# Kernel optimization log

Measured on AMD Instinct MI355X. Metric: run time of the kernel, lower is better.

Reference implementation:

```python
import jax, jax.numpy as jnp
import numpy as np
import math

N_GENES_TOTAL = 20000
N_CELLS_TOTAL = 10000
N_LATENT = 64
N_COMP = 32
SCALE_LOWER_BOUND = 1e-5
LOG_2PI = math.log(2.0 * math.pi)


def setup_inputs() -> dict:
    key = jax.random.key(0)
    ks = jax.random.split(key, 16)
    n_cells, n_genes = 512, 4000
    n_cuts, n_frags = 1000000, 1000000
    inp = {}
    inp["local_cellxgene_ix"] = jax.random.randint(ks[0], (n_frags,), 0, n_cells * n_genes)
    inp["cut_coordinates"] = jax.random.uniform(ks[1], (n_cuts,), dtype=jnp.float32)
    inp["latent"] = jax.random.normal(ks[2], (n_cells, N_LATENT), dtype=jnp.float32)
    inp["genes_oi"] = jax.random.randint(ks[3], (n_genes,), 0, N_GENES_TOTAL)
    inp["cells_oi"] = jax.random.randint(ks[4], (n_cells,), 0, N_CELLS_TOTAL)
    inp["cut_local_cellxgene_ix"] = jax.random.randint(ks[5], (n_cuts,), 0, n_cells * n_genes)
    inp["cut_local_gene_ix"] = jax.random.randint(ks[6], (n_cuts,), 0, n_genes)
    inp["n_cells"] = n_cells
    inp["n_genes"] = n_genes
    # Mixture parameters (per total gene)
    loc_init = jnp.linspace(0.0, 1.0, N_COMP + 2)[1:-1]  # (C,)
    inp["loc_w"] = jnp.broadcast_to(jax.scipy.special.logit(loc_init), (N_GENES_TOTAL, N_COMP)).astype(jnp.float32)
    inp["scale_w"] = jnp.full((N_GENES_TOTAL, N_COMP), math.log(1.0 / N_COMP / 5.0), dtype=jnp.float32)
    inp["logit_w"] = (jax.random.normal(ks[7], (N_GENES_TOTAL, N_COMP)) / math.sqrt(N_COMP)).astype(jnp.float32)
    # Decoder sparse embeddings (n_layers=0 -> input dim = n_latent)
    stdv_l = 1.0 / math.sqrt(N_LATENT)
    inp["logit_weight"] = jax.random.uniform(ks[8], (N_GENES_TOTAL, N_LATENT, N_COMP), minval=-stdv_l, maxval=stdv_l, dtype=jnp.float32)
    stdv_r = 1.0 / math.sqrt(N_LATENT) / 100.0
    inp["rho_weight"] = jax.random.uniform(ks[9], (N_GENES_TOTAL, N_LATENT), minval=-stdv_r, maxval=stdv_r, dtype=jnp.float32)
    inp["rho_bias"] = jax.random.uniform(ks[10], (N_GENES_TOTAL,), minval=1e-4, maxval=1e-2, dtype=jnp.float32)
    inp["libsize"] = jax.random.uniform(ks[11], (N_CELLS_TOTAL,), minval=1000.0, maxval=10000.0, dtype=jnp.float32)
    return inp


def reference(local_cellxgene_ix, cut_coordinates, latent, genes_oi, cells_oi,
              cut_local_cellxgene_ix, cut_local_gene_ix, n_cells, n_genes,
              loc_w, scale_w, logit_w, logit_weight, rho_weight, rho_bias, libsize):
    # Decoder (n_layers=0 => nn_output == latent)
    lw = logit_weight[genes_oi]                      # [G, L, C]
    rw = rho_weight[genes_oi]                        # [G, L]
    mixture_delta = jnp.einsum("nl,glc->ngc", latent, lw)   # [N, G, C]
    rho = latent @ rw.T                               # [N, G]

    # Gather per-cut mixture delta
    C = mixture_delta.shape[-1]
    delta = mixture_delta.reshape(-1, C)[cut_local_cellxgene_ix]  # [K, C]

    # Mixture log prob
    loc = jax.nn.sigmoid(loc_w[genes_oi])[cut_local_gene_ix]                 # [K, C]
    scale = SCALE_LOWER_BOUND + jnp.exp(scale_w[genes_oi])[cut_local_gene_ix]  # [K, C]
    logits = logit_w[genes_oi][cut_local_gene_ix] + delta                    # [K, C]
    z = (cut_coordinates[:, None] - loc) / scale
    comp_lp = -0.5 * z * z - jnp.log(scale) - 0.5 * LOG_2PI                  # Normal log_prob
    likelihood_mixture = jax.scipy.special.logsumexp(jax.nn.log_softmax(logits, axis=-1) + comp_lp, axis=-1)  # [K]

    # Fragment count Poisson likelihood
    fragmentexpression = rho_bias[genes_oi][None, :] * jnp.exp(rho) * libsize[cells_oi][:, None]  # [N, G]
    counts = jnp.zeros((n_cells * n_genes,), dtype=jnp.float32).at[local_cellxgene_ix].add(1.0).reshape(n_cells, n_genes)
    likelihood_fragmentcounts = counts * jnp.log(fragmentexpression) - fragmentexpression - jax.lax.lgamma(counts + 1.0)

    elbo = -(likelihood_mixture.sum() + likelihood_fragmentcounts.sum())
    return elbo
```

## Files before the change

kernel.cpp:

```cpp
#include <hip/hip_runtime.h>


#define TPB 256
#define CHUNK 4096
#define MAXG 4096
#define MAXN 1024
#define HALF_LOG_2PI 0.9189385332046727f

typedef short bf16x8 __attribute__((ext_vector_type(8)));
typedef float f32x4 __attribute__((ext_vector_type(4)));

static __device__ __forceinline__ unsigned short f2bf(float f) {
  unsigned u = __float_as_uint(f);
  u += 0x7fffu + ((u >> 16) & 1u);
  return (unsigned short)(u >> 16);
}

static __device__ __forceinline__ float block_reduce(float v) {
  #pragma unroll
  for (int off = 32; off > 0; off >>= 1) v += __shfl_down(v, off, 64);
  __shared__ float wsum[4];
  if ((threadIdx.x & 63) == 0) wsum[threadIdx.x >> 6] = v;
  __syncthreads();
  return (threadIdx.x == 0) ? (wsum[0] + wsum[1] + wsum[2] + wsum[3]) : 0.f;
}

__global__ __launch_bounds__(TPB) void gene_params_kernel(
    const int* __restrict__ genes_oi,
    const float* __restrict__ loc_w, const float* __restrict__ scale_w,
    const float* __restrict__ logit_w,
    const float* __restrict__ latent,
    float4* __restrict__ gp, unsigned short* __restrict__ latbf,
    int G, int NL) {
  int idx = blockIdx.x * TPB + threadIdx.x;
  int ngp = G * 32;
  if (idx < ngp) {
    int g = idx >> 5, c = idx & 31;
    long long gene = genes_oi[g];
    float lv = loc_w[gene * 32 + c];
    float loc = 1.f / (1.f + __expf(-lv));
    float sc = 1e-5f + __expf(scale_w[gene * 32 + c]);
    gp[idx] = make_float4(loc, 1.f / sc, -__logf(sc) - HALF_LOG_2PI, logit_w[gene * 32 + c]);
  } else {
    int t = idx - ngp;
    if (t < NL) latbf[t] = f2bf(latent[t]);
  }
}

__global__ __launch_bounds__(TPB) void sort_pass1(
    const int* __restrict__ cxg, const int* __restrict__ lix,
    unsigned* __restrict__ cntC, unsigned* __restrict__ cntF,
    int K, int F, unsigned G, unsigned N) {
  __shared__ unsigned hC[MAXG];
  __shared__ unsigned hF[MAXN];
  for (int t = threadIdx.x; t < MAXG; t += TPB) hC[t] = 0;
  for (int t = threadIdx.x; t < MAXN; t += TPB) hF[t] = 0;
  __syncthreads();
  int i0 = blockIdx.x * CHUNK;
  for (int t = threadIdx.x; t < CHUNK; t += TPB) {
    int i = i0 + t;
    if (i < K) { unsigned ix = (unsigned)cxg[i]; atomicAdd(&hC[ix % G], 1u); }
    if (i < F) { unsigned v = (unsigned)lix[i]; atomicAdd(&hF[v / G], 1u); }
  }
  __syncthreads();
  size_t b = blockIdx.x;
  for (unsigned t = threadIdx.x; t < G; t += TPB) cntC[b * G + t] = hC[t];
  for (unsigned t = threadIdx.x; t < N; t += TPB) cntF[b * N + t] = hF[t];
}

__global__ __launch_bounds__(TPB) void colscan_kernel(
    unsigned* __restrict__ cntC, unsigned* __restrict__ cntF,
    unsigned* __restrict__ totC, unsigned* __restrict__ totF,
    int B, unsigned G, unsigned N) {
  unsigned t = blockIdx.x * TPB + threadIdx.x;
  if (t < G) {
    unsigned run = 0;
    for (int b = 0; b < B; b++) {
      unsigned v = cntC[(size_t)b * G + t];
      cntC[(size_t)b * G + t] = run;
      run += v;
    }
    totC[t] = run;
  } else if (t < G + N) {
    unsigned s = t - G;
    unsigned run = 0;
    for (int b = 0; b < B; b++) {
      unsigned v = cntF[(size_t)b * N + s];
      cntF[(size_t)b * N + s] = run;
      run += v;
    }
    totF[s] = run;
  }
}

static __device__ void scan_dev(const unsigned* __restrict__ cnt,
                                unsigned* __restrict__ offs, int S, unsigned M) {
  __shared__ unsigned tmp[TPB];
  __shared__ unsigned base;
  if (threadIdx.x == 0) base = 0;
  __syncthreads();
  for (int c0 = 0; c0 < S; c0 += TPB) {
    int i = c0 + (int)threadIdx.x;
    unsigned v = (i < S) ? cnt[i] : 0u;
    tmp[threadIdx.x] = v;
    __syncthreads();
    for (int d = 1; d < TPB; d <<= 1) {
      unsigned t = (threadIdx.x >= (unsigned)d) ? tmp[threadIdx.x - d] : 0u;
      __syncthreads();
      tmp[threadIdx.x] += t;
      __syncthreads();
    }
    unsigned excl = tmp[threadIdx.x] - v + base;
    if (i < S) offs[i] = excl;
    __syncthreads();
    if (threadIdx.x == TPB - 1) base = excl + v;
    __syncthreads();
  }
  if (threadIdx.x == 0) offs[S] = M;
  __syncthreads();
}

__global__ __launch_bounds__(TPB) void scan2_kernel(
    const unsigned* __restrict__ totC, unsigned* __restrict__ baseC, int SC, unsigned K,
    const unsigned* __restrict__ totF, unsigned* __restrict__ baseF, int SF, unsigned F) {
  scan_dev(totC, baseC, SC, K);
  scan_dev(totF, baseF, SF, F);
}

__global__ __launch_bounds__(TPB) void sort_pass3(
    const int* __restrict__ cxg, const int* __restrict__ lix,
    const float* __restrict__ xc, const int* __restrict__ gix,
    const unsigned* __restrict__ cntC, const unsigned* __restrict__ cntF,
    const unsigned* __restrict__ baseC, const unsigned* __restrict__ baseF,
    float2* __restrict__ pl, unsigned* __restrict__ fpl,
    int K, int F, unsigned G, unsigned N) {
  __shared__ unsigned cC[MAXG];
  __shared__ unsigned cF[MAXN];
  for (int t = threadIdx.x; t < MAXG; t += TPB) cC[t] = 0;
  for (int t = threadIdx.x; t < MAXN; t += TPB) cF[t] = 0;
  __syncthreads();
  int i0 = blockIdx.x * CHUNK;
  size_t b = blockIdx.x;
  for (int t = threadIdx.x; t < CHUNK; t += TPB) {
    int i = i0 + t;
    if (i < K) {
      unsigned ix = (unsigned)cxg[i];
      unsigned g = ix % G, n = ix / G;
      unsigned r = atomicAdd(&cC[g], 1u);
      unsigned pos = baseC[g] + cntC[b * G + g] + r;
      pl[pos] = make_float2(xc[i], __uint_as_float((n << 16) | (unsigned)gix[i]));
    }
    if (i < F) {
      unsigned v = (unsigned)lix[i];
      unsigned n = v / G, g = v - n * G;
      unsigned r = atomicAdd(&cF[n], 1u);
      fpl[baseF[n] + cntF[b * N + n] + r] = (n << 16) | g;
    }
  }
}

__global__ __launch_bounds__(TPB) void cuts_v6(
    const float2* __restrict__ pl, const unsigned short* __restrict__ latbf,
    const int* __restrict__ genes_oi, const float* __restrict__ logit_weight,
    const float4* __restrict__ gp, const unsigned* __restrict__ baseC,
    float* __restrict__ partials, unsigned G) {
  const int g = blockIdx.x;
  const int lane = threadIdx.x & 63;
  const int wv = threadIdx.x >> 6;
  const int quad = lane >> 4;
  const int r16 = lane & 15;

  const float* Wb = logit_weight + (size_t)genes_oi[g] * 2048;
  bf16x8 B0a, B1a, B0b, B1b;
  #pragma unroll
  for (int j = 0; j < 8; j++) {
    int l0 = quad * 8 + j;
    B0a[j] = (short)f2bf(Wb[l0 * 32 + r16]);
    B1a[j] = (short)f2bf(Wb[(l0 + 32) * 32 + r16]);
    B0b[j] = (short)f2bf(Wb[l0 * 32 + r16 + 16]);
    B1b[j] = (short)f2bf(Wb[(l0 + 32) * 32 + r16 + 16]);
  }

  const unsigned start = baseC[g], end = baseC[g + 1];
  const unsigned ntiles = (end - start + 15) >> 4;
  float lm = 0.f;

  for (unsigned t = wv; t < ntiles; t += 4) {
    unsigned kk0 = start + t * 16;
    unsigned idx = kk0 + r16;
    float2 p = pl[idx < end ? idx : start];
    unsigned u = __float_as_uint(p.y);
    const unsigned short* lb = latbf + (size_t)(u >> 16) * 64;
    bf16x8 A0 = *(const bf16x8*)(lb + quad * 8);
    bf16x8 A1 = *(const bf16x8*)(lb + 32 + quad * 8);

    f32x4 acc0 = {0.f, 0.f, 0.f, 0.f};
    f32x4 acc1 = {0.f, 0.f, 0.f, 0.f};
    acc0 = __builtin_amdgcn_mfma_f32_16x16x32_bf16(A0, B0a, acc0, 0, 0, 0);
    acc0 = __builtin_amdgcn_mfma_f32_16x16x32_bf16(A1, B1a, acc0, 0, 0, 0);
    acc1 = __builtin_amdgcn_mfma_f32_16x16x32_bf16(A0, B0b, acc1, 0, 0, 0);
    acc1 = __builtin_amdgcn_mfma_f32_16x16x32_bf16(A1, B1b, acc1, 0, 0, 0);

    #pragma unroll
    for (int r = 0; r < 4; r++) {
      int cut = quad * 4 + r;
      float xr = __shfl(p.x, cut, 64);
      unsigned ur = (unsigned)__shfl((int)u, cut, 64);
      unsigned gi = ur & 0xffffu;
      float4 q0 = gp[(size_t)gi * 32 + r16];
      float4 q1 = gp[(size_t)gi * 32 + r16 + 16];
      float t0 = q0.w + acc0[r], t1 = q1.w + acc1[r];
      float z0 = (xr - q0.x) * q0.y, z1 = (xr - q1.x) * q1.y;
      float u0 = t0 + fmaf(-0.5f * z0, z0, q0.z);
      float u1 = t1 + fmaf(-0.5f * z1, z1, q1.z);
      float e1 = __expf(u0) + __expf(u1);
      float e2 = __expf(t0) + __expf(t1);
      #pragma unroll
      for (int d = 1; d < 16; d <<= 1) {
        e1 += __shfl_xor(e1, d, 64);
        e2 += __shfl_xor(e2, d, 64);
      }
      if (r16 == 0 && (kk0 + (unsigned)cut) < end) lm += __logf(e1) - __logf(e2);
    }
  }
  float bs = block_reduce(lm);
  if (threadIdx.x == 0) partials[blockIdx.x] = bs;
}

__global__ __launch_bounds__(TPB) void pois_v4(
    const unsigned* __restrict__ fpl, const unsigned* __restrict__ baseF,
    const float* __restrict__ latent, const int* __restrict__ genes_oi,
    const int* __restrict__ cells_oi,
    const float* __restrict__ rho_weight, const float* __restrict__ rho_bias,
    const float* __restrict__ libsize,
    float* __restrict__ partials, int N, int G) {
  int n0 = blockIdx.x * 2;
  __shared__ unsigned cnt[2 * MAXG];
  for (int t = threadIdx.x; t < 2 * MAXG; t += TPB) cnt[t] = 0;
  __shared__ __align__(16) float lat[128];
  for (int t = threadIdx.x; t < 128; t += TPB) {
    int j = t >> 6, l = t & 63;
    lat[t] = (n0 + j < N) ? latent[(size_t)(n0 + j) * 64 + l] : 0.f;
  }
  __syncthreads();
  int nhi = min(n0 + 2, N);
  unsigned s0 = baseF[n0], e0 = baseF[nhi];
  for (unsigned i = s0 + threadIdx.x; i < e0; i += TPB) {
    unsigned v = fpl[i];
    unsigned j = (v >> 16) - (unsigned)n0, g = v & 0xffffu;
    atomicAdd(&cnt[j * MAXG + g], 1u);
  }
  __syncthreads();
  float lib0 = (n0 < N) ? libsize[cells_oi[n0]] : 0.f;
  float lib1 = (n0 + 1 < N) ? libsize[cells_oi[n0 + 1]] : 0.f;
  float sum = 0.f;
  for (int g = threadIdx.x; g < G; g += TPB) {
    long long gene = genes_oi[g];
    const float4* rw = (const float4*)(rho_weight + gene * 64);
    float r0 = 0.f, r1 = 0.f;
    #pragma unroll
    for (int i = 0; i < 16; i++) {
      float4 wv = rw[i];
      float4 l0 = *(const float4*)(&lat[i * 4]);
      float4 l1 = *(const float4*)(&lat[64 + i * 4]);
      r0 = fmaf(wv.x, l0.x, r0); r0 = fmaf(wv.y, l0.y, r0);
      r0 = fmaf(wv.z, l0.z, r0); r0 = fmaf(wv.w, l0.w, r0);
      r1 = fmaf(wv.x, l1.x, r1); r1 = fmaf(wv.y, l1.y, r1);
      r1 = fmaf(wv.z, l1.z, r1); r1 = fmaf(wv.w, l1.w, r1);
    }
    float rb = rho_bias[gene];
    if (n0 < N) {
      float fe = rb * __expf(r0) * lib0;
      unsigned c = cnt[g];
      float term = -fe;
      if (c) {
        float lf = 0.f;
        for (unsigned q2 = 2; q2 <= c; q2++) lf += __logf((float)q2);
        term += (float)c * __logf(fe) - lf;
      }
      sum += term;
    }
    if (n0 + 1 < N) {
      float fe = rb * __expf(r1) * lib1;
      unsigned c = cnt[MAXG + g];
      float term = -fe;
      if (c) {
        float lf = 0.f;
        for (unsigned q2 = 2; q2 <= c; q2++) lf += __logf((float)q2);
        term += (float)c * __logf(fe) - lf;
      }
      sum += term;
    }
  }
  float bs = block_reduce(sum);
  if (threadIdx.x == 0) partials[blockIdx.x] = bs;
}

__global__ __launch_bounds__(TPB) void finalize_kernel(
    const float* __restrict__ p1, int n1,
    const float* __restrict__ p2, int n2, float* __restrict__ out) {
  float s = 0.f;
  for (int i = threadIdx.x; i < n1; i += TPB) s += p1[i];
  for (int i = threadIdx.x; i < n2; i += TPB) s += p2[i];
  float bs = block_reduce(s);
  if (threadIdx.x == 0) out[0] = -bs;
}

extern "C" void kernel_launch(void* const* d_in, const int* in_sizes, int n_in,
                              void* d_out, int out_size, void* d_ws, size_t ws_size,
                              hipStream_t stream) {
  const int*   lix          = (const int*)d_in[0];
  const float* xc           = (const float*)d_in[1];
  const float* latent       = (const float*)d_in[2];
  const int*   genes_oi     = (const int*)d_in[3];
  const int*   cells_oi     = (const int*)d_in[4];
  const int*   cxg          = (const int*)d_in[5];
  const int*   gix          = (const int*)d_in[6];
  const float* loc_w        = (const float*)d_in[9];
  const float* scale_w      = (const float*)d_in[10];
  const float* logit_w      = (const float*)d_in[11];
  const float* logit_weight = (const float*)d_in[12];
  const float* rho_weight   = (const float*)d_in[13];
  const float* rho_bias     = (const float*)d_in[14];
  const float* libsize      = (const float*)d_in[15];
  float* out = (float*)d_out;

  const int F = in_sizes[0];
  const int K = in_sizes[1];
  const int N = in_sizes[2] / 64;
  const int G = in_sizes[3];
  const int NL = N * 64;

  const int M = (K > F) ? K : F;
  const int B = (M + CHUNK - 1) / CHUNK;
  const int PB = (N + 1) / 2;

  size_t off = 0;
  auto alloc = [&](size_t bytes) {
    size_t o = off;
    off = (off + bytes + 255) & ~(size_t)255;
    return o;
  };
  size_t cntC_off  = alloc((size_t)B * G * 4);
  size_t cntF_off  = alloc((size_t)B * N * 4);
  size_t totC_off  = alloc((size_t)G * 4);
  size_t totF_off  = alloc((size_t)N * 4);
  size_t baseC_off = alloc((size_t)(G + 1) * 4);
  size_t baseF_off = alloc((size_t)(N + 1) * 4);
  size_t pl_off    = alloc((size_t)K * 8);
  size_t fpl_off   = alloc((size_t)F * 4);
  size_t gp_off    = alloc((size_t)G * 32 * 16);
  size_t lb_off    = alloc((size_t)NL * 2);
  size_t p1_off    = alloc((size_t)G * 4);
  size_t p2_off    = alloc((size_t)PB * 4);
  (void)ws_size;

  char* ws = (char*)d_ws;
  unsigned* cntC  = (unsigned*)(ws + cntC_off);
  unsigned* cntF  = (unsigned*)(ws + cntF_off);
  unsigned* totC  = (unsigned*)(ws + totC_off);
  unsigned* totF  = (unsigned*)(ws + totF_off);
  unsigned* baseC = (unsigned*)(ws + baseC_off);
  unsigned* baseF = (unsigned*)(ws + baseF_off);
  float2*   pl    = (float2*)(ws + pl_off);
  unsigned* fpl   = (unsigned*)(ws + fpl_off);
  float4*   gp    = (float4*)(ws + gp_off);
  unsigned short* latbf = (unsigned short*)(ws + lb_off);
  float*    p1    = (float*)(ws + p1_off);
  float*    p2    = (float*)(ws + p2_off);

  gene_params_kernel<<<(G * 32 + NL + TPB - 1) / TPB, TPB, 0, stream>>>(
      genes_oi, loc_w, scale_w, logit_w, latent, gp, latbf, G, NL);
  sort_pass1<<<B, TPB, 0, stream>>>(cxg, lix, cntC, cntF, K, F, (unsigned)G, (unsigned)N);
  colscan_kernel<<<(G + N + TPB - 1) / TPB, TPB, 0, stream>>>(
      cntC, cntF, totC, totF, B, (unsigned)G, (unsigned)N);
  scan2_kernel<<<1, TPB, 0, stream>>>(totC, baseC, G, (unsigned)K, totF, baseF, N, (unsigned)F);
  sort_pass3<<<B, TPB, 0, stream>>>(cxg, lix, xc, gix, cntC, cntF, baseC, baseF,
                                    pl, fpl, K, F, (unsigned)G, (unsigned)N);
  cuts_v6<<<G, TPB, 0, stream>>>(pl, latbf, genes_oi, logit_weight, gp, baseC, p1, (unsigned)G);
  pois_v4<<<PB, TPB, 0, stream>>>(fpl, baseF, latent, genes_oi, cells_oi,
                                  rho_weight, rho_bias, libsize, p2, N, G);
  finalize_kernel<<<1, TPB, 0, stream>>>(p1, G, p2, PB, out);
}
```

Measured before the change: 533.6 us.

## Merge prep kernels, wave-parallel scans, and fold finalize into Poisson kernel

Fuses the gene-parameter/latent-conversion kernel into the first histogram pass as extra blocks, and rewrites the column scan so one wavefront scans each column with shuffles instead of one serial thread. The global scan now uses one wavefront per array with shuffle scans in place of a barrier-heavy block scan. The final reduction kernel is removed: the last Poisson block, found through an atomic ticket, sums all partials. This cuts kernel launches and serial scan latency, at the cost of a ticket reset and threadfence ordering.

```diff
diff --git a/kernel.cpp b/kernel.cpp
--- a/kernel.cpp
+++ b/kernel.cpp
@@ -25,32 +25,29 @@
   return (threadIdx.x == 0) ? (wsum[0] + wsum[1] + wsum[2] + wsum[3]) : 0.f;
 }
 
-__global__ __launch_bounds__(TPB) void gene_params_kernel(
+__global__ __launch_bounds__(TPB) void prep_hist_kernel(
+    const int* __restrict__ cxg, const int* __restrict__ lix,
+    unsigned* __restrict__ cntC, unsigned* __restrict__ cntF,
     const int* __restrict__ genes_oi,
     const float* __restrict__ loc_w, const float* __restrict__ scale_w,
-    const float* __restrict__ logit_w,
-    const float* __restrict__ latent,
+    const float* __restrict__ logit_w, const float* __restrict__ latent,
     float4* __restrict__ gp, unsigned short* __restrict__ latbf,
-    int G, int NL) {
-  int idx = blockIdx.x * TPB + threadIdx.x;
-  int ngp = G * 32;
-  if (idx < ngp) {
-    int g = idx >> 5, c = idx & 31;
-    long long gene = genes_oi[g];
-    float lv = loc_w[gene * 32 + c];
-    float loc = 1.f / (1.f + __expf(-lv));
-    float sc = 1e-5f + __expf(scale_w[gene * 32 + c]);
-    gp[idx] = make_float4(loc, 1.f / sc, -__logf(sc) - HALF_LOG_2PI, logit_w[gene * 32 + c]);
-  } else {
-    int t = idx - ngp;
-    if (t < NL) latbf[t] = f2bf(latent[t]);
-  }
-}
-
-__global__ __launch_bounds__(TPB) void sort_pass1(
-    const int* __restrict__ cxg, const int* __restrict__ lix,
-    unsigned* __restrict__ cntC, unsigned* __restrict__ cntF,
-    int K, int F, unsigned G, unsigned N) {
+    int K, int F, unsigned G, unsigned N, int B, int NL) {
+  if ((int)blockIdx.x >= B) {
+    int idx = ((int)blockIdx.x - B) * TPB + threadIdx.x;
+    int ngp = (int)G * 32;
+    if (idx < ngp) {
+      int g = idx >> 5, c = idx & 31;
+      long long gene = genes_oi[g];
+      float lv = loc_w[gene * 32 + c];
+      float loc = 1.f / (1.f + __expf(-lv));
+      float sc = 1e-5f + __expf(scale_w[gene * 32 + c]);
+      gp[idx] = make_float4(loc, 1.f / sc, -__logf(sc) - HALF_LOG_2PI, logit_w[gene * 32 + c]);
+    } else if (idx - ngp < NL) {
+      latbf[idx - ngp] = f2bf(latent[idx - ngp]);
+    }
+    return;
+  }
   __shared__ unsigned hC[MAXG];
   __shared__ unsigned hF[MAXN];
   for (int t = threadIdx.x; t < MAXG; t += TPB) hC[t] = 0;
@@ -68,63 +65,73 @@
   for (unsigned t = threadIdx.x; t < N; t += TPB) cntF[b * N + t] = hF[t];
 }
 
-__global__ __launch_bounds__(TPB) void colscan_kernel(
+__global__ __launch_bounds__(TPB) void colscan_v2(
     unsigned* __restrict__ cntC, unsigned* __restrict__ cntF,
     unsigned* __restrict__ totC, unsigned* __restrict__ totF,
     int B, unsigned G, unsigned N) {
-  unsigned t = blockIdx.x * TPB + threadIdx.x;
-  if (t < G) {
-    unsigned run = 0;
-    for (int b = 0; b < B; b++) {
-      unsigned v = cntC[(size_t)b * G + t];
-      cntC[(size_t)b * G + t] = run;
-      run += v;
-    }
-    totC[t] = run;
-  } else if (t < G + N) {
-    unsigned s = t - G;
-    unsigned run = 0;
-    for (int b = 0; b < B; b++) {
-      unsigned v = cntF[(size_t)b * N + s];
-      cntF[(size_t)b * N + s] = run;
-      run += v;
-    }
-    totF[s] = run;
-  }
-}
-
-static __device__ void scan_dev(const unsigned* __restrict__ cnt,
-                                unsigned* __restrict__ offs, int S, unsigned M) {
-  __shared__ unsigned tmp[TPB];
-  __shared__ unsigned base;
-  if (threadIdx.x == 0) base = 0;
-  __syncthreads();
-  for (int c0 = 0; c0 < S; c0 += TPB) {
-    int i = c0 + (int)threadIdx.x;
-    unsigned v = (i < S) ? cnt[i] : 0u;
-    tmp[threadIdx.x] = v;
-    __syncthreads();
-    for (int d = 1; d < TPB; d <<= 1) {
-      unsigned t = (threadIdx.x >= (unsigned)d) ? tmp[threadIdx.x - d] : 0u;
-      __syncthreads();
-      tmp[threadIdx.x] += t;
-      __syncthreads();
-    }
-    unsigned excl = tmp[threadIdx.x] - v + base;
-    if (i < S) offs[i] = excl;
-    __syncthreads();
-    if (threadIdx.x == TPB - 1) base = excl + v;
-    __syncthreads();
-  }
-  if (threadIdx.x == 0) offs[S] = M;
-  __syncthreads();
-}
-
-__global__ __launch_bounds__(TPB) void scan2_kernel(
+  unsigned wid = blockIdx.x * 4 + (threadIdx.x >> 6);
+  int lane = threadIdx.x & 63;
+  if (wid >= G + N) return;
+  unsigned* col;
+  unsigned stride;
+  unsigned* tot;
+  if (wid < G) { col = cntC + wid; stride = G; tot = totC + wid; }
+  else         { col = cntF + (wid - G); stride = N; tot = totF + (wid - G); }
+  unsigned base = 0;
+  for (int b0 = 0; b0 < B; b0 += 64) {
+    int b = b0 + lane;
+    unsigned v = (b < B) ? col[(size_t)b * stride] : 0u;
+    unsigned inc = v;
+    #pragma unroll
+    for (int d = 1; d < 64; d <<= 1) {
+      unsigned t2 = __shfl_up(inc, d, 64);
+      if (lane >= d) inc += t2;
+    }
+    if (b < B) col[(size_t)b * stride] = inc - v + base;
+    base += __shfl(inc, 63, 64);
+  }
+  if (lane == 0) *tot = base;
+}
+
+__global__ __launch_bounds__(TPB) void scan2_v2(
     const unsigned* __restrict__ totC, unsigned* __restrict__ baseC, int SC, unsigned K,
-    const unsigned* __restrict__ totF, unsigned* __restrict__ baseF, int SF, unsigned F) {
-  scan_dev(totC, baseC, SC, K);
-  scan_dev(totF, baseF, SF, F);
+    const unsigned* __restrict__ totF, unsigned* __restrict__ baseF, int SF, unsigned F,
+    unsigned* __restrict__ ticket) {
+  int lane = threadIdx.x & 63;
+  int wv = threadIdx.x >> 6;
+  if (wv == 0) {
+    unsigned base = 0;
+    for (int i0 = 0; i0 < SC; i0 += 64) {
+      int i = i0 + lane;
+      unsigned v = (i < SC) ? totC[i] : 0u;
+      unsigned inc = v;
+      #pragma unroll
+      for (int d = 1; d < 64; d <<= 1) {
+        unsigned t = __shfl_up(inc, d, 64);
+        if (lane >= d) inc += t;
+      }
+      if (i < SC) baseC[i] = inc - v + base;
+      base += __shfl(inc, 63, 64);
+    }
+    if (lane == 0) baseC[SC] = K;
+  } else if (wv == 1) {
+    unsigned base = 0;
+    for (int i0 = 0; i0 < SF; i0 += 64) {
+      int i = i0 + lane;
+      unsigned v = (i < SF) ? totF[i] : 0u;
+      unsigned inc = v;
+      #pragma unroll
+      for (int d = 1; d < 64; d <<= 1) {
+        unsigned t = __shfl_up(inc, d, 64);
+        if (lane >= d) inc += t;
+      }
+      if (i < SF) baseF[i] = inc - v + base;
+      base += __shfl(inc, 63, 64);
+    }
+    if (lane == 0) baseF[SF] = F;
+  } else if (threadIdx.x == 128) {
+    *ticket = 0u;
+  }
 }
 
 __global__ __launch_bounds__(TPB) void sort_pass3(
@@ -227,14 +234,17 @@
   if (threadIdx.x == 0) partials[blockIdx.x] = bs;
 }
 
-__global__ __launch_bounds__(TPB) void pois_v4(
+__global__ __launch_bounds__(TPB) void pois_v5(
     const unsigned* __restrict__ fpl, const unsigned* __restrict__ baseF,
     const float* __restrict__ latent, const int* __restrict__ genes_oi,
     const int* __restrict__ cells_oi,
     const float* __restrict__ rho_weight, const float* __restrict__ rho_bias,
     const float* __restrict__ libsize,
-    float* __restrict__ partials, int N, int G) {
+    float* __restrict__ p1, int n1,
+    float* __restrict__ p2, unsigned* __restrict__ ticket,
+    float* __restrict__ out, int N, int G) {
   int n0 = blockIdx.x * 2;
+  const int PB = gridDim.x;
   __shared__ unsigned cnt[2 * MAXG];
   for (int t = threadIdx.x; t < 2 * MAXG; t += TPB) cnt[t] = 0;
   __shared__ __align__(16) float lat[128];
@@ -293,17 +303,21 @@
     }
   }
   float bs = block_reduce(sum);
-  if (threadIdx.x == 0) partials[blockIdx.x] = bs;
-}
-
-__global__ __launch_bounds__(TPB) void finalize_kernel(
-    const float* __restrict__ p1, int n1,
-    const float* __restrict__ p2, int n2, float* __restrict__ out) {
-  float s = 0.f;
-  for (int i = threadIdx.x; i < n1; i += TPB) s += p1[i];
-  for (int i = threadIdx.x; i < n2; i += TPB) s += p2[i];
-  float bs = block_reduce(s);
-  if (threadIdx.x == 0) out[0] = -bs;
+  __shared__ unsigned slast;
+  if (threadIdx.x == 0) {
+    p2[blockIdx.x] = bs;
+    __threadfence();
+    slast = atomicAdd(ticket, 1u);
+  }
+  __syncthreads();
+  if (slast == (unsigned)(PB - 1)) {
+    __threadfence();
+    float s = 0.f;
+    for (int i = threadIdx.x; i < n1; i += TPB) s += p1[i];
+    for (int i = threadIdx.x; i < PB; i += TPB) s += p2[i];
+    float tot = block_reduce(s);
+    if (threadIdx.x == 0) out[0] = -tot;
+  }
 }
 
 extern "C" void kernel_launch(void* const* d_in, const int* in_sizes, int n_in,
@@ -334,6 +348,7 @@
   const int M = (K > F) ? K : F;
   const int B = (M + CHUNK - 1) / CHUNK;
   const int PB = (N + 1) / 2;
+  const int GPB = (G * 32 + NL + TPB - 1) / TPB;
 
   size_t off = 0;
   auto alloc = [&](size_t bytes) {
@@ -353,6 +368,7 @@
   size_t lb_off    = alloc((size_t)NL * 2);
   size_t p1_off    = alloc((size_t)G * 4);
   size_t p2_off    = alloc((size_t)PB * 4);
+  size_t tk_off    = alloc(4);
   (void)ws_size;
 
   char* ws = (char*)d_ws;
@@ -368,17 +384,19 @@
   unsigned short* latbf = (unsigned short*)(ws + lb_off);
   float*    p1    = (float*)(ws + p1_off);
   float*    p2    = (float*)(ws + p2_off);
-
-  gene_params_kernel<<<(G * 32 + NL + TPB - 1) / TPB, TPB, 0, stream>>>(
-      genes_oi, loc_w, scale_w, logit_w, latent, gp, latbf, G, NL);
-  sort_pass1<<<B, TPB, 0, stream>>>(cxg, lix, cntC, cntF, K, F, (unsigned)G, (unsigned)N);
-  colscan_kernel<<<(G + N + TPB - 1) / TPB, TPB, 0, stream>>>(
+  unsigned* ticket = (unsigned*)(ws + tk_off);
+
+  prep_hist_kernel<<<B + GPB, TPB, 0, stream>>>(
+      cxg, lix, cntC, cntF, genes_oi, loc_w, scale_w, logit_w, latent,
+      gp, latbf, K, F, (unsigned)G, (unsigned)N, B, NL);
+  colscan_v2<<<(G + N + 3) / 4, TPB, 0, stream>>>(
       cntC, cntF, totC, totF, B, (unsigned)G, (unsigned)N);
-  scan2_kernel<<<1, TPB, 0, stream>>>(totC, baseC, G, (unsigned)K, totF, baseF, N, (unsigned)F);
+  scan2_v2<<<1, TPB, 0, stream>>>(totC, baseC, G, (unsigned)K,
+                                  totF, baseF, N, (unsigned)F, ticket);
   sort_pass3<<<B, TPB, 0, stream>>>(cxg, lix, xc, gix, cntC, cntF, baseC, baseF,
                                     pl, fpl, K, F, (unsigned)G, (unsigned)N);
   cuts_v6<<<G, TPB, 0, stream>>>(pl, latbf, genes_oi, logit_weight, gp, baseC, p1, (unsigned)G);
-  pois_v4<<<PB, TPB, 0, stream>>>(fpl, baseF, latent, genes_oi, cells_oi,
-                                  rho_weight, rho_bias, libsize, p2, N, G);
-  finalize_kernel<<<1, TPB, 0, stream>>>(p1, G, p2, PB, out);
-}
+  pois_v5<<<PB, TPB, 0, stream>>>(fpl, baseF, latent, genes_oi, cells_oi,
+                                  rho_weight, rho_bias, libsize,
+                                  p1, G, p2, ticket, out, N, G);
+}
```

Result: faster. 447.8 us (-16.1%).
